# Kernel tuning notes

Measured on AMD Instinct MI355X. Metric: run time of the kernel, lower is better.

## Reference

```python
import jax, jax.numpy as jnp
import numpy as np

B, T, H, O, P, L = 128, 64, 512, 47, 4, 3
G = 4 * H


def setup_inputs() -> dict:
    key = jax.random.key(0)
    k = jax.random.split(key, 10)
    s = 0.05
    return {
        "x": jax.random.randint(k[0], (B, T), 0, O),
        "properties": jax.random.normal(k[1], (B, P), jnp.float32),
        "enc_w": jax.random.normal(k[2], (H, O), jnp.float32) * s,
        "enc_b": jnp.zeros((H,), jnp.float32),
        "dec_w": jax.random.normal(k[3], (O, H), jnp.float32) * s,
        "dec_b": jnp.zeros((O,), jnp.float32),
        "w_ih0": jax.random.normal(k[4], (G, H + P), jnp.float32) * s,
        "w_hh0": jax.random.normal(k[5], (G, H), jnp.float32) * s,
        "b_ih0": jnp.zeros((G,), jnp.float32).at[H:2 * H].set(1.0),
        "b_hh0": jnp.zeros((G,), jnp.float32).at[H:2 * H].set(1.0),
        "w_ih_rest": jax.random.normal(k[6], (L - 1, G, H), jnp.float32) * s,
        "w_hh_rest": jax.random.normal(k[7], (L - 1, G, H), jnp.float32) * s,
        "b_ih_rest": jnp.zeros((L - 1, G), jnp.float32).at[:, H:2 * H].set(1.0),
        "b_hh_rest": jnp.zeros((L - 1, G), jnp.float32).at[:, H:2 * H].set(1.0),
    }


def _lstm_cell(x, h, c, w_ih, w_hh, b_ih, b_hh):
    # torch gate order: i, f, g, o
    g = x @ w_ih.T + h @ w_hh.T + (b_ih + b_hh)
    i, f, gg, o = jnp.split(g, 4, axis=-1)
    c = jax.nn.sigmoid(f) * c + jax.nn.sigmoid(i) * jnp.tanh(gg)
    h = jax.nn.sigmoid(o) * jnp.tanh(c)
    return h, c


def reference(x, properties, enc_w, enc_b, dec_w, dec_b,
              w_ih0, w_hh0, b_ih0, b_hh0,
              w_ih_rest, w_hh_rest, b_ih_rest, b_hh_rest):
    batch = properties.shape[0]
    max_len = x.shape[1]
    n_layers = w_ih_rest.shape[0] + 1
    hidden = w_hh0.shape[1]
    out_size = dec_w.shape[0]

    # initial one-hot on symbol 1 (start token), encoded
    init = jnp.zeros((batch, out_size), properties.dtype).at[:, 1].set(1.0)
    inputs0 = init @ enc_w.T + enc_b  # [B, H]
    h0 = jnp.zeros((n_layers, batch, hidden), properties.dtype)
    c0 = jnp.zeros_like(h0)

    def step(carry, _):
        h, c, inp = carry
        xcat = jnp.concatenate([inp, properties], axis=1)  # [B, H+P]
        hs, cs = [], []
        hh, cc = _lstm_cell(xcat, h[0], c[0], w_ih0, w_hh0, b_ih0, b_hh0)
        hs.append(hh); cs.append(cc)
        for l in range(n_layers - 1):
            hh, cc = _lstm_cell(hh, h[l + 1], c[l + 1],
                                w_ih_rest[l], w_hh_rest[l],
                                b_ih_rest[l], b_hh_rest[l])
            hs.append(hh); cs.append(cc)
        logits = hh @ dec_w.T + dec_b          # [B, O]
        nxt = logits @ enc_w.T + enc_b         # feed logits back through encoder
        return (jnp.stack(hs), jnp.stack(cs), nxt), logits

    _, logits_seq = jax.lax.scan(step, (h0, c0, inputs0), None, length=max_len)
    return jnp.transpose(logits_seq, (1, 0, 2))  # [B, T, O]
```

## Files before the change

kernel.cpp:

```cpp
#include <hip/hip_runtime.h>
#include <hip/hip_fp16.h>
#include <math.h>

#define B 128
#define T 64
#define H 512
#define O 47
#define PP 4
#define G 2048
#define GH (G*H)
#define HB (H*B)


typedef _Float16 h16;
typedef _Float16 h16x2 __attribute__((ext_vector_type(2)));

__device__ __forceinline__ unsigned int pack2h(float a, float b) {
    union { unsigned int u; h16 h[2]; } c;
    c.h[0] = (h16)a; c.h[1] = (h16)b;
    return c.u;
}
__device__ __forceinline__ h16x2 as_h2(unsigned int u) {
    union { unsigned int u; h16x2 v; } c; c.u = u; return c.v;
}
__device__ __forceinline__ uint2 cload_u2(const unsigned int* p) {
    unsigned long long v = __hip_atomic_load((const unsigned long long*)p,
                                             __ATOMIC_RELAXED, __HIP_MEMORY_SCOPE_AGENT);
    union { unsigned long long u; uint2 w; } c; c.u = v; return c.w;
}
__device__ __forceinline__ void cstore_u2(unsigned int* p, uint2 v) {
    union { unsigned long long u; uint2 w; } c; c.w = v;
    __hip_atomic_store((unsigned long long*)p, c.u,
                       __ATOMIC_RELAXED, __HIP_MEMORY_SCOPE_AGENT);
}
#define FDOT2(w, x, c) __builtin_amdgcn_fdot2(as_h2(w), as_h2(x), (c), false)

#define SM_WH     0
#define SM_BIAS   12288
#define SM_DECH   14336
#define SM_BL     14592
#define SM_G      14608
#define SM_DB     22800
#define SM_H      23824
#define SM_TOTAL  24080

#define HSLOT   32768
#define NSLOT   65
#define HTOT    (3 * NSLOT * HSLOT)
#define OFF_C   HTOT
#define OFF_M   (OFF_C + 3*HB)
#define OFF_W0  (OFF_M + 4*HB)
#define OFF_BA  (OFF_W0 + 16*HB)
#define OFF_BB  (OFF_BA + 4*HB)
#define OFF_DV  (OFF_BB + 4*HB)
#define OFF_BAR (OFF_DV + 5120)
#define NEED_A  ((size_t)(OFF_BAR + 4160) * sizeof(float))

struct RnnParams {
  const float* w_hh0;
  const float* w_ihr;
  const float* w_hhr;
  const float* b_ihr;
  const float* b_hhr;
  const float* dec_w;
  const float* dec_b;
  const float* W0eff;
  const float* biasA;
  const float* biasB;
  unsigned int* h;
  float* c;
  float* out;
  unsigned int* arrive;
  unsigned int* gocnt;
};


__global__ __launch_bounds__(256) void k_init_a(
    const float* __restrict__ enc_w, const float* __restrict__ enc_b,
    const float* __restrict__ dec_b,
    unsigned int* __restrict__ h, float* __restrict__ c,
    float* __restrict__ d, float* __restrict__ nxt0,
    unsigned int* __restrict__ barptr)
{
    int idx = blockIdx.x * 256 + threadIdx.x;
    if (idx < 4160) barptr[idx] = 0u;
    if (idx < HSLOT) {
        #pragma unroll
        for (int l = 0; l < 3; ++l) h[(size_t)l * NSLOT * HSLOT + idx] = 0u;
    }
    #pragma unroll
    for (int i = 0; i < 3; ++i) c[i*HB + idx] = 0.f;
    if (idx < H) {
        float s = 0.f;
        for (int o = 0; o < O; ++o) s += enc_w[idx*O + o] * dec_b[o];
        d[idx] = enc_b[idx] + s;
        nxt0[idx] = enc_w[idx*O + 1] + enc_b[idx];
    }
}

__global__ __launch_bounds__(256) void k_init_b(
    const float* __restrict__ enc_w, const float* __restrict__ enc_b,
    const float* __restrict__ dec_b,
    float* __restrict__ h, float* __restrict__ c,
    float* __restrict__ d, float* __restrict__ nxt0,
    unsigned int* __restrict__ barptr)
{
    int idx = blockIdx.x * 256 + threadIdx.x;
    if (idx < 4160) barptr[idx] = 0u;
    #pragma unroll
    for (int i = 0; i < 3; ++i) h[i*HB + idx] = 0.f;
    #pragma unroll
    for (int i = 0; i < 3; ++i) c[i*HB + idx] = 0.f;
    if (idx < H) {
        float s = 0.f;
        for (int o = 0; o < O; ++o) s += enc_w[idx*O + o] * dec_b[o];
        d[idx] = enc_b[idx] + s;
        nxt0[idx] = enc_w[idx*O + 1] + enc_b[idx];
    }
}

__global__ __launch_bounds__(256) void k_M(
    const float* __restrict__ enc_w, const float* __restrict__ dec_w,
    float* __restrict__ M)
{
    int idx = blockIdx.x * 256 + threadIdx.x;
    int hh = idx >> 9, k = idx & 511;
    float s = 0.f;
    for (int o = 0; o < O; ++o) s += enc_w[hh*O + o] * dec_w[o*H + k];
    M[hh*H + k] = s;
}

__global__ __launch_bounds__(256) void k_cd(
    const float* __restrict__ w_ih0,
    const float* __restrict__ nxt0, const float* __restrict__ d,
    float* __restrict__ x0c, float* __restrict__ cd)
{
    int j = blockIdx.x * 256 + threadIdx.x;
    const float* row = w_ih0 + (size_t)j * (H + PP);
    float sA = 0.f, sB = 0.f;
    for (int k = 0; k < H; ++k) { float w = row[k]; sA += w * nxt0[k]; sB += w * d[k]; }
    x0c[j] = sA; cd[j] = sB;
}

__global__ __launch_bounds__(256) void k_W0eff(
    const float* __restrict__ w_ih0, const float* __restrict__ M,
    float* __restrict__ W0eff)
{
    int k0 = (threadIdx.x & 127) * 4;
    int jsub = threadIdx.x >> 7;
    int j0 = blockIdx.x * 16 + jsub * 8;
    float4 a[8];
    #pragma unroll
    for (int i = 0; i < 8; ++i) a[i] = make_float4(0.f, 0.f, 0.f, 0.f);
    for (int hh = 0; hh < H; ++hh) {
        float4 mv = *(const float4*)(M + (size_t)hh * H + k0);
        #pragma unroll
        for (int i = 0; i < 8; ++i) {
            float w = w_ih0[(size_t)(j0 + i) * (H + PP) + hh];
            a[i].x += w * mv.x; a[i].y += w * mv.y;
            a[i].z += w * mv.z; a[i].w += w * mv.w;
        }
    }
    #pragma unroll
    for (int i = 0; i < 8; ++i)
        *(float4*)(W0eff + (size_t)(j0 + i) * H + k0) = a[i];
}

__global__ __launch_bounds__(256) void k_bias(
    const float* __restrict__ w_ih0, const float* __restrict__ props,
    const float* __restrict__ b_ih0, const float* __restrict__ b_hh0,
    const float* __restrict__ x0c, const float* __restrict__ cd,
    float* __restrict__ biasA, float* __restrict__ biasB)
{
    int idx = blockIdx.x * 256 + threadIdx.x;
    int j = idx >> 7, b = idx & 127;
    const float* wp = w_ih0 + (size_t)j * (H + PP) + H;
    const float* pr = props + b * PP;
    float pc = wp[0]*pr[0] + wp[1]*pr[1] + wp[2]*pr[2] + wp[3]*pr[3];
    float base = b_ih0[j] + b_hh0[j] + pc;
    biasA[idx] = base + x0c[j];
    biasB[idx] = base + cd[j];
}


__device__ __forceinline__ void stage_weights(
    unsigned int* sWH, float* sBias, unsigned int* sDecH, float* sBL,
    const RnnParams& p, int wg, int u0, int tid, bool isdec)
{
    const float* bases[6] = { p.W0eff, p.w_hh0, p.w_ihr, p.w_hhr,
                              p.w_ihr + GH, p.w_hhr + GH };
    #pragma unroll
    for (int s = 0; s < 6; ++s) {
        for (int idx = tid; idx < 2048; idx += 512) {
            int r = idx >> 8, kp = idx & 255;
            int j = (r >> 1) * H + u0 + (r & 1);
            const float* src = bases[s] + (size_t)j * H + 2*kp;
            sWH[s*2048 + (r << 8) + kp] = pack2h(src[0], src[1]);
        }
    }
    for (int idx = tid; idx < 2048; idx += 512) {
        int pl = idx >> 10, r = (idx >> 7) & 7, b = idx & 127;
        int j = (r >> 1) * H + u0 + (r & 1);
        sBias[idx] = (pl ? p.biasB : p.biasA)[(size_t)j * B + b];
    }
    if (tid < 16) {
        int l = tid >> 3, r = tid & 7;
        int j = (r >> 1) * H + u0 + (r & 1);
        sBL[tid] = p.b_ihr[l*G + j] + p.b_hhr[l*G + j];
    }
    if (isdec && tid < 256) {
        const float* src = p.dec_w + (size_t)wg * H + 2*tid;
        sDecH[tid] = pack2h(src[0], src[1]);
    }
}


__global__ __launch_bounds__(512, 2) void rnn_persistent_a(RnnParams p)
{
    extern __shared__ float sm[];
    const int tid   = threadIdx.x;
    const int wg    = blockIdx.x;
    const int u0    = wg * 2;
    const int b4    = tid & 31;
    const int khalf = (tid >> 5) & 1;
    const int ks    = tid >> 6;

    unsigned int* sWH   = (unsigned int*)(sm + SM_WH);
    float*        sBias = sm + SM_BIAS;
    unsigned int* sDecH = (unsigned int*)(sm + SM_DECH);
    float*        sBL   = sm + SM_BL;
    float*        sG    = sm + SM_G;
    float*        sDb   = sm + SM_DB;
    float*        sH    = sm + SM_H;

    float* c0 = p.c; float* c1 = p.c + HB; float* c2 = p.c + 2*HB;
    const bool  isdec = (wg < O);
    const float decb  = isdec ? p.dec_b[wg] : 0.f;

    __builtin_amdgcn_fence(__ATOMIC_ACQUIRE, "agent");

    stage_weights(sWH, sBias, sDecH, sBL, p, wg, u0, tid, isdec);
    __syncthreads();

    unsigned int epoch = 0;
    unsigned int* arrive = p.arrive;
    unsigned int* gocnt  = p.gocnt;

    auto gbar = [&]() {
        ++epoch;
        __syncthreads();
        if (tid == 0)
            __hip_atomic_fetch_add(&arrive[(size_t)wg * 16], 1u,
                                   __ATOMIC_RELEASE, __HIP_MEMORY_SCOPE_AGENT);
        if (wg == 0) {
            if (tid < 256) {
                while (__hip_atomic_load(&arrive[(size_t)tid * 16],
                        __ATOMIC_RELAXED, __HIP_MEMORY_SCOPE_AGENT) < epoch)
                    __builtin_amdgcn_s_sleep(1);
            }
            __syncthreads();
            if (tid == 0)
                __hip_atomic_fetch_add(gocnt, 1u,
                                       __ATOMIC_RELEASE, __HIP_MEMORY_SCOPE_AGENT);
        }
        if (tid == 0) {
            while (__hip_atomic_load(gocnt, __ATOMIC_RELAXED,
                                     __HIP_MEMORY_SCOPE_AGENT) < epoch)
                __builtin_amdgcn_s_sleep(1);
        }
        __syncthreads();
    };

    auto slot = [&](int l, int s) -> unsigned int* {
        return p.h + ((size_t)(l * NSLOT + s) << 15);
    };

    auto phase = [&](const unsigned int* __restrict__ xs,
                     const unsigned int* __restrict__ hs,
                     int ph, const float* biasPlane, const float* biasScal,
                     float* cc, unsigned int* hout, bool dopig, float* dout) {
        float4 acc[8];
        #pragma unroll
        for (int r = 0; r < 8; ++r) acc[r] = make_float4(0.f, 0.f, 0.f, 0.f);
        float4 accd = make_float4(0.f, 0.f, 0.f, 0.f);

        const unsigned int* wx = sWH + (ph*2 + 0) * 2048;
        const unsigned int* wh = sWH + (ph*2 + 1) * 2048;
        const int kp0 = ks * 32 + khalf * 16;
        const int xo  = 4 * b4;

        for (int kp = kp0; kp < kp0 + 16; kp += 4) {
            uint4 x0 = *(const uint4*)(xs + (kp+0)*128 + xo);
            uint4 x1 = *(const uint4*)(xs + (kp+1)*128 + xo);
            uint4 x2 = *(const uint4*)(xs + (kp+2)*128 + xo);
            uint4 x3 = *(const uint4*)(xs + (kp+3)*128 + xo);
            #pragma unroll
            for (int r = 0; r < 8; ++r) {
                uint4 wq = *(const uint4*)(wx + r*256 + kp);
                acc[r].x = FDOT2(wq.x, x0.x, acc[r].x); acc[r].y = FDOT2(wq.x, x0.y, acc[r].y);
                acc[r].z = FDOT2(wq.x, x0.z, acc[r].z); acc[r].w = FDOT2(wq.x, x0.w, acc[r].w);
                acc[r].x = FDOT2(wq.y, x1.x, acc[r].x); acc[r].y = FDOT2(wq.y, x1.y, acc[r].y);
                acc[r].z = FDOT2(wq.y, x1.z, acc[r].z); acc[r].w = FDOT2(wq.y, x1.w, acc[r].w);
                acc[r].x = FDOT2(wq.z, x2.x, acc[r].x); acc[r].y = FDOT2(wq.z, x2.y, acc[r].y);
                acc[r].z = FDOT2(wq.z, x2.z, acc[r].z); acc[r].w = FDOT2(wq.z, x2.w, acc[r].w);
                acc[r].x = FDOT2(wq.w, x3.x, acc[r].x); acc[r].y = FDOT2(wq.w, x3.y, acc[r].y);
                acc[r].z = FDOT2(wq.w, x3.z, acc[r].z); acc[r].w = FDOT2(wq.w, x3.w, acc[r].w);
            }
            if (dopig) {
                uint4 dq = *(const uint4*)(sDecH + kp);
                accd.x = FDOT2(dq.x, x0.x, accd.x); accd.y = FDOT2(dq.x, x0.y, accd.y);
                accd.z = FDOT2(dq.x, x0.z, accd.z); accd.w = FDOT2(dq.x, x0.w, accd.w);
                accd.x = FDOT2(dq.y, x1.x, accd.x); accd.y = FDOT2(dq.y, x1.y, accd.y);
                accd.z = FDOT2(dq.y, x1.z, accd.z); accd.w = FDOT2(dq.y, x1.w, accd.w);
                accd.x = FDOT2(dq.z, x2.x, accd.x); accd.y = FDOT2(dq.z, x2.y, accd.y);
                accd.z = FDOT2(dq.z, x2.z, accd.z); accd.w = FDOT2(dq.z, x2.w, accd.w);
                accd.x = FDOT2(dq.w, x3.x, accd.x); accd.y = FDOT2(dq.w, x3.y, accd.y);
                accd.z = FDOT2(dq.w, x3.z, accd.z); accd.w = FDOT2(dq.w, x3.w, accd.w);
            }
        }
        for (int kp = kp0; kp < kp0 + 16; kp += 4) {
            uint4 x0 = *(const uint4*)(hs + (kp+0)*128 + xo);
            uint4 x1 = *(const uint4*)(hs + (kp+1)*128 + xo);
            uint4 x2 = *(const uint4*)(hs + (kp+2)*128 + xo);
            uint4 x3 = *(const uint4*)(hs + (kp+3)*128 + xo);
            #pragma unroll
            for (int r = 0; r < 8; ++r) {
                uint4 wq = *(const uint4*)(wh + r*256 + kp);
                acc[r].x = FDOT2(wq.x, x0.x, acc[r].x); acc[r].y = FDOT2(wq.x, x0.y, acc[r].y);
                acc[r].z = FDOT2(wq.x, x0.z, acc[r].z); acc[r].w = FDOT2(wq.x, x0.w, acc[r].w);
                acc[r].x = FDOT2(wq.y, x1.x, acc[r].x); acc[r].y = FDOT2(wq.y, x1.y, acc[r].y);
                acc[r].z = FDOT2(wq.y, x1.z, acc[r].z); acc[r].w = FDOT2(wq.y, x1.w, acc[r].w);
                acc[r].x = FDOT2(wq.z, x2.x, acc[r].x); acc[r].y = FDOT2(wq.z, x2.y, acc[r].y);
                acc[r].z = FDOT2(wq.z, x2.z, acc[r].z); acc[r].w = FDOT2(wq.z, x2.w, acc[r].w);
                acc[r].x = FDOT2(wq.w, x3.x, acc[r].x); acc[r].y = FDOT2(wq.w, x3.y, acc[r].y);
                acc[r].z = FDOT2(wq.w, x3.z, acc[r].z); acc[r].w = FDOT2(wq.w, x3.w, acc[r].w);
            }
        }

        #pragma unroll
        for (int r = 0; r < 8; ++r) {
            acc[r].x += __shfl_xor(acc[r].x, 32, 64);
            acc[r].y += __shfl_xor(acc[r].y, 32, 64);
            acc[r].z += __shfl_xor(acc[r].z, 32, 64);
            acc[r].w += __shfl_xor(acc[r].w, 32, 64);
        }
        if (khalf == 0) {
            #pragma unroll
            for (int r = 0; r < 8; ++r)
                *(float4*)(sG + ((r*8 + ks)*32 + b4)*4) = acc[r];
        }
        if (dopig) {
            accd.x += __shfl_xor(accd.x, 32, 64);
            accd.y += __shfl_xor(accd.y, 32, 64);
            accd.z += __shfl_xor(accd.z, 32, 64);
            accd.w += __shfl_xor(accd.w, 32, 64);
            if (khalf == 0) *(float4*)(sDb + (ks*32 + b4)*4) = accd;
        }
        __syncthreads();

        if (tid < 256) {
            int mi = tid >> 7, b = tid & 127;
            float g[4];
            #pragma unroll
            for (int q = 0; q < 4; ++q) {
                int r = q*2 + mi;
                float s = biasPlane ? biasPlane[r*128 + b] : biasScal[r];
                #pragma unroll
                for (int k2 = 0; k2 < 8; ++k2)
                    s += sG[((r*8 + k2)*32 + (b >> 2))*4 + (b & 3)];
                g[q] = s;
            }
            float ig = 1.f/(1.f+expf(-g[0]));
            float fg = 1.f/(1.f+expf(-g[1]));
            float gv = tanhf(g[2]);
            float og = 1.f/(1.f+expf(-g[3]));
            int idx = (u0 + mi)*B + b;
            float cn = fg*cc[idx] + ig*gv;
            cc[idx] = cn;
            sH[mi*128 + b] = og*tanhf(cn);
        } else if (dopig && tid < 384) {
            int b = tid - 256;
            float s = decb;
            #pragma unroll
            for (int k2 = 0; k2 < 8; ++k2)
                s += sDb[(k2*32 + (b >> 2))*4 + (b & 3)];
            dout[(size_t)b * (T*O)] = s;
        }
        __syncthreads();
        if (tid < 64) {
            int b0 = tid * 2;
            uint2 v;
            v.x = pack2h(sH[b0],     sH[128 + b0]);
            v.y = pack2h(sH[b0 + 1], sH[128 + b0 + 1]);
            cstore_u2(hout + wg*128 + b0, v);
        }
    };

    for (int t = 0; t < T; ++t) {
        bool pig = (t > 0) && isdec;
        phase(slot(2, t), slot(0, t), 0, sBias + (t == 0 ? 0 : 1024), nullptr,
              c0, slot(0, t+1), pig,
              pig ? (p.out + (size_t)(t-1)*O + wg) : nullptr);
        gbar();
        phase(slot(0, t+1), slot(1, t), 1, nullptr, sBL, c1, slot(1, t+1),
              false, nullptr);
        gbar();
        phase(slot(1, t+1), slot(2, t), 2, nullptr, sBL + 8, c2, slot(2, t+1),
              false, nullptr);
        gbar();
    }

    if (isdec) {
        const unsigned int* xs = slot(2, T);
        float4 accd = make_float4(0.f, 0.f, 0.f, 0.f);
        const int kp0 = ks * 32 + khalf * 16;
        const int xo  = 4 * b4;
        for (int kp = kp0; kp < kp0 + 16; kp += 4) {
            uint4 x0 = *(const uint4*)(xs + (kp+0)*128 + xo);
            uint4 x1 = *(const uint4*)(xs + (kp+1)*128 + xo);
            uint4 x2 = *(const uint4*)(xs + (kp+2)*128 + xo);
            uint4 x3 = *(const uint4*)(xs + (kp+3)*128 + xo);
            uint4 dq = *(const uint4*)(sDecH + kp);
            accd.x = FDOT2(dq.x, x0.x, accd.x); accd.y = FDOT2(dq.x, x0.y, accd.y);
            accd.z = FDOT2(dq.x, x0.z, accd.z); accd.w = FDOT2(dq.x, x0.w, accd.w);
            accd.x = FDOT2(dq.y, x1.x, accd.x); accd.y = FDOT2(dq.y, x1.y, accd.y);
            accd.z = FDOT2(dq.y, x1.z, accd.z); accd.w = FDOT2(dq.y, x1.w, accd.w);
            accd.x = FDOT2(dq.z, x2.x, accd.x); accd.y = FDOT2(dq.z, x2.y, accd.y);
            accd.z = FDOT2(dq.z, x2.z, accd.z); accd.w = FDOT2(dq.z, x2.w, accd.w);
            accd.x = FDOT2(dq.w, x3.x, accd.x); accd.y = FDOT2(dq.w, x3.y, accd.y);
            accd.z = FDOT2(dq.w, x3.z, accd.z); accd.w = FDOT2(dq.w, x3.w, accd.w);
        }
        accd.x += __shfl_xor(accd.x, 32, 64);
        accd.y += __shfl_xor(accd.y, 32, 64);
        accd.z += __shfl_xor(accd.z, 32, 64);
        accd.w += __shfl_xor(accd.w, 32, 64);
        if (khalf == 0) *(float4*)(sDb + (ks*32 + b4)*4) = accd;
    }
    __syncthreads();
    if (isdec && tid < 128) {
        int b = tid;
        float s = decb;
        #pragma unroll
        for (int k2 = 0; k2 < 8; ++k2)
            s += sDb[(k2*32 + (b >> 2))*4 + (b & 3)];
        p.out[((size_t)b * T + 63) * O + wg] = s;
    }
}


__global__ __launch_bounds__(512, 2) void rnn_persistent_b(RnnParams p)
{
    extern __shared__ float sm[];
    const int tid = threadIdx.x;
    const int wg  = blockIdx.x;
    const int u0  = wg * 2;
    const int b2  = tid & 63;
    const int ks  = tid >> 6;

    unsigned int* sWH   = (unsigned int*)(sm + SM_WH);
    float*        sBias = sm + SM_BIAS;
    unsigned int* sDecH = (unsigned int*)(sm + SM_DECH);
    float*        sBL   = sm + SM_BL;
    float2*       sGbuf = (float2*)(sm + SM_G);
    float2*       sDecb = (float2*)(sm + SM_DB);
    float*        sH    = sm + SM_H;

    unsigned int* h0p = p.h + 0*32768; unsigned int* h0c = p.h + 1*32768;
    unsigned int* h1p = p.h + 2*32768; unsigned int* h1c = p.h + 3*32768;
    unsigned int* h2p = p.h + 4*32768; unsigned int* h2c = p.h + 5*32768;
    float* c0 = p.c; float* c1 = p.c + HB; float* c2 = p.c + 2*HB;

    const bool  isdec = (wg < O);
    const float decb  = isdec ? p.dec_b[wg] : 0.f;

    stage_weights(sWH, sBias, sDecH, sBL, p, wg, u0, tid, isdec);
    __syncthreads();

    unsigned int epoch = 0;
    unsigned int* arrive = p.arrive;
    unsigned int* gocnt  = p.gocnt;
    auto gbar = [&]() {
        ++epoch;
        __syncthreads();
        if (tid == 0)
            __hip_atomic_fetch_add(&arrive[(size_t)wg * 16], 1u,
                                   __ATOMIC_RELEASE, __HIP_MEMORY_SCOPE_AGENT);
        if (wg == 0) {
            if (tid < 256) {
                while (__hip_atomic_load(&arrive[(size_t)tid * 16],
                        __ATOMIC_RELAXED, __HIP_MEMORY_SCOPE_AGENT) < epoch)
                    __builtin_amdgcn_s_sleep(1);
            }
            __syncthreads();
            if (tid == 0)
                __hip_atomic_fetch_add(gocnt, 1u,
                                       __ATOMIC_RELEASE, __HIP_MEMORY_SCOPE_AGENT);
        }
        if (tid == 0) {
            while (__hip_atomic_load(gocnt, __ATOMIC_RELAXED,
                                     __HIP_MEMORY_SCOPE_AGENT) < epoch)
                __builtin_amdgcn_s_sleep(1);
        }
        __syncthreads();
    };

    auto phase = [&](const unsigned int* __restrict__ xs,
                     const unsigned int* __restrict__ hs,
                     int ph, const float* biasPlane, const float* biasScal,
                     float* cc, unsigned int* hout, bool dopig, float* dout) {
        float2 acc[8];
        #pragma unroll
        for (int r = 0; r < 8; ++r) { acc[r].x = 0.f; acc[r].y = 0.f; }
        float2 accd; accd.x = 0.f; accd.y = 0.f;

        const unsigned int* wx = sWH + (ph*2 + 0) * 2048;
        const unsigned int* wh = sWH + (ph*2 + 1) * 2048;
        const int kb = ks * 32;
        const int xo = 2 * b2;

        for (int kp = kb; kp < kb + 32; kp += 4) {
            uint2 x0 = cload_u2(xs + (kp+0)*128 + xo);
            uint2 x1 = cload_u2(xs + (kp+1)*128 + xo);
            uint2 x2 = cload_u2(xs + (kp+2)*128 + xo);
            uint2 x3 = cload_u2(xs + (kp+3)*128 + xo);
            if (dopig) {
                uint4 dq = *(const uint4*)(sDecH + kp);
                accd.x = FDOT2(dq.x, x0.x, accd.x); accd.y = FDOT2(dq.x, x0.y, accd.y);
                accd.x = FDOT2(dq.y, x1.x, accd.x); accd.y = FDOT2(dq.y, x1.y, accd.y);
                accd.x = FDOT2(dq.z, x2.x, accd.x); accd.y = FDOT2(dq.z, x2.y, accd.y);
                accd.x = FDOT2(dq.w, x3.x, accd.x); accd.y = FDOT2(dq.w, x3.y, accd.y);
            }
            #pragma unroll
            for (int r = 0; r < 8; ++r) {
                uint4 wq = *(const uint4*)(wx + r*256 + kp);
                acc[r].x = FDOT2(wq.x, x0.x, acc[r].x); acc[r].y = FDOT2(wq.x, x0.y, acc[r].y);
                acc[r].x = FDOT2(wq.y, x1.x, acc[r].x); acc[r].y = FDOT2(wq.y, x1.y, acc[r].y);
                acc[r].x = FDOT2(wq.z, x2.x, acc[r].x); acc[r].y = FDOT2(wq.z, x2.y, acc[r].y);
                acc[r].x = FDOT2(wq.w, x3.x, acc[r].x); acc[r].y = FDOT2(wq.w, x3.y, acc[r].y);
            }
        }
        for (int kp = kb; kp < kb + 32; kp += 4) {
            uint2 x0 = cload_u2(hs + (kp+0)*128 + xo);
            uint2 x1 = cload_u2(hs + (kp+1)*128 + xo);
            uint2 x2 = cload_u2(hs + (kp+2)*128 + xo);
            uint2 x3 = cload_u2(hs + (kp+3)*128 + xo);
            #pragma unroll
            for (int r = 0; r < 8; ++r) {
                uint4 wq = *(const uint4*)(wh + r*256 + kp);
                acc[r].x = FDOT2(wq.x, x0.x, acc[r].x); acc[r].y = FDOT2(wq.x, x0.y, acc[r].y);
                acc[r].x = FDOT2(wq.y, x1.x, acc[r].x); acc[r].y = FDOT2(wq.y, x1.y, acc[r].y);
                acc[r].x = FDOT2(wq.z, x2.x, acc[r].x); acc[r].y = FDOT2(wq.z, x2.y, acc[r].y);
                acc[r].x = FDOT2(wq.w, x3.x, acc[r].x); acc[r].y = FDOT2(wq.w, x3.y, acc[r].y);
            }
        }

        #pragma unroll
        for (int r = 0; r < 8; ++r) sGbuf[(r*8 + ks)*64 + b2] = acc[r];
        if (dopig) sDecb[ks*64 + b2] = accd;
        __syncthreads();

        if (tid < 256) {
            int mi = tid >> 7, b = tid & 127;
            float g[4];
            #pragma unroll
            for (int q = 0; q < 4; ++q) {
                int r = q*2 + mi;
                float s = biasPlane ? biasPlane[r*128 + b] : biasScal[r];
                #pragma unroll
                for (int k2 = 0; k2 < 8; ++k2) {
                    float2 v = sGbuf[(r*8 + k2)*64 + (b >> 1)];
                    s += (b & 1) ? v.y : v.x;
                }
                g[q] = s;
            }
            float ig = 1.f/(1.f+expf(-g[0]));
            float fg = 1.f/(1.f+expf(-g[1]));
            float gv = tanhf(g[2]);
            float og = 1.f/(1.f+expf(-g[3]));
            int idx = (u0 + mi)*B + b;
            float cn = fg*cc[idx] + ig*gv;
            cc[idx] = cn;
            sH[mi*128 + b] = og*tanhf(cn);
        } else if (dopig && tid < 384) {
            int b = tid - 256;
            float s = decb;
            #pragma unroll
            for (int k2 = 0; k2 < 8; ++k2) {
                float2 v = sDecb[k2*64 + (b >> 1)];
                s += (b & 1) ? v.y : v.x;
            }
            dout[(size_t)b * (T*O)] = s;
        }
        __syncthreads();
        if (tid < 64) {
            int b0 = tid * 2;
            uint2 v;
            v.x = pack2h(sH[b0],     sH[128 + b0]);
            v.y = pack2h(sH[b0 + 1], sH[128 + b0 + 1]);
            cstore_u2(hout + wg*128 + b0, v);
        }
    };

    for (int t = 0; t < T; ++t) {
        bool pig = (t > 0) && isdec;
        phase(h2p, h0p, 0, sBias + (t == 0 ? 0 : 1024), nullptr,
              c0, h0c, pig, pig ? (p.out + (size_t)(t-1)*O + wg) : nullptr);
        gbar();
        phase(h0c, h1p, 1, nullptr, sBL, c1, h1c, false, nullptr);
        gbar();
        phase(h1c, h2p, 2, nullptr, sBL + 8, c2, h2c, false, nullptr);
        gbar();
        unsigned int* tp;
        tp = h0p; h0p = h0c; h0c = tp;
        tp = h1p; h1p = h1c; h1c = tp;
        tp = h2p; h2p = h2c; h2c = tp;
    }

    if (isdec) {
        float2 accd; accd.x = 0.f; accd.y = 0.f;
        const int kb = ks * 32;
        const int xo = 2 * b2;
        for (int kp = kb; kp < kb + 32; kp += 4) {
            uint2 x0 = cload_u2(h2p + (kp+0)*128 + xo);
            uint2 x1 = cload_u2(h2p + (kp+1)*128 + xo);
            uint2 x2 = cload_u2(h2p + (kp+2)*128 + xo);
            uint2 x3 = cload_u2(h2p + (kp+3)*128 + xo);
            uint4 dq = *(const uint4*)(sDecH + kp);
            accd.x = FDOT2(dq.x, x0.x, accd.x); accd.y = FDOT2(dq.x, x0.y, accd.y);
            accd.x = FDOT2(dq.y, x1.x, accd.x); accd.y = FDOT2(dq.y, x1.y, accd.y);
            accd.x = FDOT2(dq.z, x2.x, accd.x); accd.y = FDOT2(dq.z, x2.y, accd.y);
            accd.x = FDOT2(dq.w, x3.x, accd.x); accd.y = FDOT2(dq.w, x3.y, accd.y);
        }
        sDecb[ks*64 + b2] = accd;
    }
    __syncthreads();
    if (isdec && tid < 128) {
        int b = tid;
        float s = decb;
        #pragma unroll
        for (int k2 = 0; k2 < 8; ++k2) {
            float2 v = sDecb[k2*64 + (b >> 1)];
            s += (b & 1) ? v.y : v.x;
        }
        p.out[((size_t)b * T + 63) * O + wg] = s;
    }
}


__global__ __launch_bounds__(256) void init_kernel(
    const float* __restrict__ enc_w, const float* __restrict__ enc_b,
    float* __restrict__ nxtT, float* __restrict__ hbufs, float* __restrict__ cbufs)
{
    int idx = blockIdx.x * 256 + threadIdx.x;
    #pragma unroll
    for (int i = 0; i < 6; ++i) hbufs[i * HB + idx] = 0.f;
    #pragma unroll
    for (int i = 0; i < 3; ++i) cbufs[i * HB + idx] = 0.f;
    int h = idx >> 7;
    nxtT[idx] = enc_w[h * O + 1] + enc_b[h];
}

__global__ __launch_bounds__(256) void transpose_kernel(
    const float* __restrict__ dec_w, const float* __restrict__ enc_w,
    float* __restrict__ dec_wT, float* __restrict__ enc_wT)
{
    int idx = blockIdx.x * 256 + threadIdx.x;
    if (idx < O * H) {
        int o = idx / H, k = idx - o * H;
        dec_wT[k * O + o] = dec_w[o * H + k];
        enc_wT[o * H + k] = enc_w[k * O + o];
    }
}

__global__ __launch_bounds__(512) void gates_kernel(
    const float* __restrict__ xT, const float* __restrict__ hT,
    const float* __restrict__ w_ih, int ldih,
    const float* __restrict__ w_hh,
    const float* __restrict__ b_ih, const float* __restrict__ b_hh,
    const float* __restrict__ props,
    float* __restrict__ c, float* __restrict__ hout)
{
    const int wg = blockIdx.x;
    const int bg = wg >> 7, jg = wg & 127;
    const int m0 = jg * 4;
    const int lane_b = threadIdx.x & 63, ks = threadIdx.x >> 6;
    const int bb = (bg << 6) + lane_b;
    float acc[16];
    #pragma unroll
    for (int r = 0; r < 16; ++r) acc[r] = 0.f;
    const float* wih_rows[16]; const float* whh_rows[16];
    #pragma unroll
    for (int q = 0; q < 4; ++q)
        #pragma unroll
        for (int mi = 0; mi < 4; ++mi) {
            int r = q * 4 + mi, j = q * H + m0 + mi;
            wih_rows[r] = w_ih + (size_t)j * ldih;
            whh_rows[r] = w_hh + (size_t)j * H;
        }
    const int kbeg = ks * 64, kend = ks * 64 + 64;
    for (int k0 = kbeg; k0 < kend; k0 += 4) {
        float x0 = xT[(k0+0)*B+bb], x1 = xT[(k0+1)*B+bb];
        float x2 = xT[(k0+2)*B+bb], x3 = xT[(k0+3)*B+bb];
        #pragma unroll
        for (int r = 0; r < 16; ++r) {
            float4 wv = *(const float4*)(wih_rows[r] + k0);
            acc[r] += wv.x*x0 + wv.y*x1 + wv.z*x2 + wv.w*x3;
        }
    }
    for (int k0 = kbeg; k0 < kend; k0 += 4) {
        float x0 = hT[(k0+0)*B+bb], x1 = hT[(k0+1)*B+bb];
        float x2 = hT[(k0+2)*B+bb], x3 = hT[(k0+3)*B+bb];
        #pragma unroll
        for (int r = 0; r < 16; ++r) {
            float4 wv = *(const float4*)(whh_rows[r] + k0);
            acc[r] += wv.x*x0 + wv.y*x1 + wv.z*x2 + wv.w*x3;
        }
    }
    __shared__ float gbuf[16][8][64];
    #pragma unroll
    for (int r = 0; r < 16; ++r) gbuf[r][ks][lane_b] = acc[r];
    __syncthreads();
    if (threadIdx.x < 256) {
        int mi = threadIdx.x >> 6, b = threadIdx.x & 63;
        int bbo = (bg << 6) + b, m = m0 + mi;
        float g[4];
        #pragma unroll
        for (int q = 0; q < 4; ++q) {
            int j = q * H + m;
            float s = b_ih[j] + b_hh[j];
            #pragma unroll
            for (int k2 = 0; k2 < 8; ++k2) s += gbuf[q*4+mi][k2][b];
            if (props) {
                const float* wp = w_ih + (size_t)j * ldih + H;
                const float* pp = props + bbo * PP;
                s += wp[0]*pp[0] + wp[1]*pp[1] + wp[2]*pp[2] + wp[3]*pp[3];
            }
            g[q] = s;
        }
        float ig = 1.f/(1.f+expf(-g[0]));
        float fg = 1.f/(1.f+expf(-g[1]));
        float gv = tanhf(g[2]);
        float og = 1.f/(1.f+expf(-g[3]));
        int idx = m * B + bbo;
        float cn = fg * c[idx] + ig * gv;
        c[idx] = cn;
        hout[idx] = og * tanhf(cn);
    }
}

__global__ __launch_bounds__(256) void decenc_kernel(
    const float* __restrict__ h2T, const float* __restrict__ dec_wT,
    const float* __restrict__ dec_b, const float* __restrict__ enc_wT,
    const float* __restrict__ enc_b, float* __restrict__ nxtT,
    float* __restrict__ out, int t)
{
    const int b = blockIdx.x;
    const int w = threadIdx.x >> 6, o = threadIdx.x & 63;
    __shared__ float red[4][64];
    __shared__ float lg[64];
    float p = 0.f;
    if (o < O)
        for (int k = w * 128; k < w * 128 + 128; ++k)
            p += h2T[k * B + b] * dec_wT[k * O + o];
    red[w][o] = p;
    __syncthreads();
    if (threadIdx.x < 64) {
        int oo = threadIdx.x;
        float s = 0.f;
        if (oo < O) {
            s = dec_b[oo] + red[0][oo] + red[1][oo] + red[2][oo] + red[3][oo];
            out[((size_t)b * T + t) * O + oo] = s;
        }
        lg[oo] = s;
    }
    __syncthreads();
    for (int h = threadIdx.x; h < H; h += 256) {
        float s = enc_b[h];
        #pragma unroll 1
        for (int oo = 0; oo < O; ++oo) s += lg[oo] * enc_wT[oo * H + h];
        nxtT[h * B + b] = s;
    }
}

extern "C" void kernel_launch(void* const* d_in, const int* in_sizes, int n_in,
                              void* d_out, int out_size, void* d_ws, size_t ws_size,
                              hipStream_t stream) {
    const float* props = (const float*)d_in[1];
    const float* enc_w = (const float*)d_in[2];
    const float* enc_b = (const float*)d_in[3];
    const float* dec_w = (const float*)d_in[4];
    const float* dec_b = (const float*)d_in[5];
    const float* w_ih0 = (const float*)d_in[6];
    const float* w_hh0 = (const float*)d_in[7];
    const float* b_ih0 = (const float*)d_in[8];
    const float* b_hh0 = (const float*)d_in[9];
    const float* w_ihr = (const float*)d_in[10];
    const float* w_hhr = (const float*)d_in[11];
    const float* b_ihr = (const float*)d_in[12];
    const float* b_hhr = (const float*)d_in[13];

    float* ws = (float*)d_ws;
    const size_t NEED_B = ((size_t)34 * HB + 5120 + 4160) * sizeof(float);
    const size_t LDS_BYTES = (size_t)SM_TOTAL * sizeof(float);

    static int lds_a = -1, lds_b = -1;
    if (lds_a < 0) {
        lds_a = (hipFuncSetAttribute((const void*)rnn_persistent_a,
                  hipFuncAttributeMaxDynamicSharedMemorySize,
                  (int)LDS_BYTES) == hipSuccess) ? 1 : 0;
        lds_b = (hipFuncSetAttribute((const void*)rnn_persistent_b,
                  hipFuncAttributeMaxDynamicSharedMemorySize,
                  (int)LDS_BYTES) == hipSuccess) ? 1 : 0;
    }

    if (ws_size >= NEED_A && lds_a == 1) {
        unsigned int* hbuf = (unsigned int*)ws;
        float* cbuf  = ws + OFF_C;
        float* M     = ws + OFF_M;
        float* W0eff = ws + OFF_W0;
        float* biasA = ws + OFF_BA;
        float* biasB = ws + OFF_BB;
        float* dvec  = ws + OFF_DV;
        float* nxt0  = dvec + 512;
        float* x0c   = nxt0 + 512;
        float* cd    = x0c + 2048;
        unsigned int* barptr = (unsigned int*)(ws + OFF_BAR);

        k_init_a<<<256, 256, 0, stream>>>(enc_w, enc_b, dec_b, hbuf, cbuf,
                                          dvec, nxt0, barptr);
        k_M<<<1024, 256, 0, stream>>>(enc_w, dec_w, M);
        k_cd<<<8, 256, 0, stream>>>(w_ih0, nxt0, dvec, x0c, cd);
        k_W0eff<<<128, 256, 0, stream>>>(w_ih0, M, W0eff);
        k_bias<<<1024, 256, 0, stream>>>(w_ih0, props, b_ih0, b_hh0, x0c, cd,
                                         biasA, biasB);

        RnnParams prm;
        prm.w_hh0 = w_hh0; prm.w_ihr = w_ihr; prm.w_hhr = w_hhr;
        prm.b_ihr = b_ihr; prm.b_hhr = b_hhr;
        prm.dec_w = dec_w; prm.dec_b = dec_b;
        prm.W0eff = W0eff; prm.biasA = biasA; prm.biasB = biasB;
        prm.h = hbuf; prm.c = cbuf; prm.out = (float*)d_out;
        prm.arrive = barptr; prm.gocnt = barptr + 4096;

        void* args[] = { &prm };
        hipLaunchCooperativeKernel((const void*)rnn_persistent_a,
                                   dim3(256), dim3(512), args,
                                   (unsigned int)LDS_BYTES, stream);
        return;
    }

    if (ws_size >= NEED_B && lds_b == 1) {
        unsigned int* hbuf = (unsigned int*)ws;
        float* cbuf  = ws + 3*HB;
        float* M     = ws + 6*HB;
        float* W0eff = ws + 10*HB;
        float* biasA = ws + 26*HB;
        float* biasB = ws + 30*HB;
        float* dvec  = ws + 34*HB;
        float* nxt0  = dvec + 512;
        float* x0c   = nxt0 + 512;
        float* cd    = x0c + 2048;
        unsigned int* barptr = (unsigned int*)(cd + 2048);

        k_init_b<<<256, 256, 0, stream>>>(enc_w, enc_b, dec_b, (float*)hbuf,
                                          cbuf, dvec, nxt0, barptr);
        k_M<<<1024, 256, 0, stream>>>(enc_w, dec_w, M);
        k_cd<<<8, 256, 0, stream>>>(w_ih0, nxt0, dvec, x0c, cd);
        k_W0eff<<<128, 256, 0, stream>>>(w_ih0, M, W0eff);
        k_bias<<<1024, 256, 0, stream>>>(w_ih0, props, b_ih0, b_hh0, x0c, cd,
                                         biasA, biasB);

        RnnParams prm;
        prm.w_hh0 = w_hh0; prm.w_ihr = w_ihr; prm.w_hhr = w_hhr;
        prm.b_ihr = b_ihr; prm.b_hhr = b_hhr;
        prm.dec_w = dec_w; prm.dec_b = dec_b;
        prm.W0eff = W0eff; prm.biasA = biasA; prm.biasB = biasB;
        prm.h = hbuf; prm.c = cbuf; prm.out = (float*)d_out;
        prm.arrive = barptr; prm.gocnt = barptr + 4096;

        void* args[] = { &prm };
        hipLaunchCooperativeKernel((const void*)rnn_persistent_b,
                                   dim3(256), dim3(512), args,
                                   (unsigned int)LDS_BYTES, stream);
        return;
    }

    float* nxtT   = ws;
    float* hb     = ws + HB;
    float* cb     = ws + 7*HB;
    float* dec_wT = ws + 10*HB;
    float* enc_wT = dec_wT + H*O;

    init_kernel<<<256, 256, 0, stream>>>(enc_w, enc_b, nxtT, hb, cb);
    transpose_kernel<<<(O*H + 255)/256, 256, 0, stream>>>(dec_w, enc_w, dec_wT, enc_wT);

    float* hprev[3]; float* hcur[3];
    for (int l = 0; l < 3; ++l) { hprev[l] = hb + (2*l)*HB; hcur[l] = hb + (2*l+1)*HB; }

    for (int t = 0; t < T; ++t) {
        gates_kernel<<<256, 512, 0, stream>>>(nxtT, hprev[0], w_ih0, H+PP, w_hh0,
                                              b_ih0, b_hh0, props, cb, hcur[0]);
        gates_kernel<<<256, 512, 0, stream>>>(hcur[0], hprev[1], w_ihr, H, w_hhr,
                                              b_ihr, b_hhr, nullptr, cb + HB, hcur[1]);
        gates_kernel<<<256, 512, 0, stream>>>(hcur[1], hprev[2], w_ihr + (size_t)G*H, H,
                                              w_hhr + (size_t)G*H, b_ihr + G, b_hhr + G,
                                              nullptr, cb + 2*HB, hcur[2]);
        decenc_kernel<<<B, 256, 0, stream>>>(hcur[2], dec_wT, dec_b, enc_wT, enc_b,
                                             nxtT, (float*)d_out, t);
        for (int l = 0; l < 3; ++l) { float* tp = hprev[l]; hprev[l] = hcur[l]; hcur[l] = tp; }
    }
}
```

Before: 2.323 ms.

## Split grid barrier into arrive/wait and overlap recurrent matmul with barrier

Replaces the centralized two-level grid barrier (workgroup 0 gathers arrivals, then releases everyone through a go counter) with a split arrive/wait barrier in which every workgroup polls all 256 arrival counters itself. Each phase now computes the recurrent h·W_hh part before waiting, since it only depends on the previous timestep's state, and does the input part and gate math after the wait. This moves independent work into the barrier latency and removes one round trip through workgroup 0. The cost is that every workgroup polls 256 counters, which adds atomic traffic, and correctness now relies on the slot layout keeping previous-step state valid during the wait.

```diff
diff --git a/kernel.cpp b/kernel.cpp
--- a/kernel.cpp
+++ b/kernel.cpp
@@ -242,53 +242,64 @@
     stage_weights(sWH, sBias, sDecH, sBL, p, wg, u0, tid, isdec);
     __syncthreads();
 
-    unsigned int epoch = 0;
+    unsigned int done = 0;
     unsigned int* arrive = p.arrive;
-    unsigned int* gocnt  = p.gocnt;
-
-    auto gbar = [&]() {
-        ++epoch;
+
+    auto bar_wait = [&]() {
+        if (tid < 256) {
+            while (__hip_atomic_load(&arrive[(size_t)tid * 16],
+                    __ATOMIC_RELAXED, __HIP_MEMORY_SCOPE_AGENT) < done)
+                __builtin_amdgcn_s_sleep(1);
+        }
+        __syncthreads();
+    };
+    auto bar_arrive = [&]() {
         __syncthreads();
         if (tid == 0)
             __hip_atomic_fetch_add(&arrive[(size_t)wg * 16], 1u,
                                    __ATOMIC_RELEASE, __HIP_MEMORY_SCOPE_AGENT);
-        if (wg == 0) {
-            if (tid < 256) {
-                while (__hip_atomic_load(&arrive[(size_t)tid * 16],
-                        __ATOMIC_RELAXED, __HIP_MEMORY_SCOPE_AGENT) < epoch)
-                    __builtin_amdgcn_s_sleep(1);
-            }
-            __syncthreads();
-            if (tid == 0)
-                __hip_atomic_fetch_add(gocnt, 1u,
-                                       __ATOMIC_RELEASE, __HIP_MEMORY_SCOPE_AGENT);
-        }
-        if (tid == 0) {
-            while (__hip_atomic_load(gocnt, __ATOMIC_RELAXED,
-                                     __HIP_MEMORY_SCOPE_AGENT) < epoch)
-                __builtin_amdgcn_s_sleep(1);
-        }
-        __syncthreads();
+        ++done;
     };
 
     auto slot = [&](int l, int s) -> unsigned int* {
         return p.h + ((size_t)(l * NSLOT + s) << 15);
     };
 
-    auto phase = [&](const unsigned int* __restrict__ xs,
-                     const unsigned int* __restrict__ hs,
-                     int ph, const float* biasPlane, const float* biasScal,
-                     float* cc, unsigned int* hout, bool dopig, float* dout) {
-        float4 acc[8];
+    const int kp0 = ks * 32 + khalf * 16;
+    const int xo  = 4 * b4;
+
+    float4 acc[8];
+
+    auto h_part = [&](const unsigned int* __restrict__ hs, int ph) {
         #pragma unroll
         for (int r = 0; r < 8; ++r) acc[r] = make_float4(0.f, 0.f, 0.f, 0.f);
+        const unsigned int* wh = sWH + (ph*2 + 1) * 2048;
+        for (int kp = kp0; kp < kp0 + 16; kp += 4) {
+            uint4 x0 = *(const uint4*)(hs + (kp+0)*128 + xo);
+            uint4 x1 = *(const uint4*)(hs + (kp+1)*128 + xo);
+            uint4 x2 = *(const uint4*)(hs + (kp+2)*128 + xo);
+            uint4 x3 = *(const uint4*)(hs + (kp+3)*128 + xo);
+            #pragma unroll
+            for (int r = 0; r < 8; ++r) {
+                uint4 wq = *(const uint4*)(wh + r*256 + kp);
+                acc[r].x = FDOT2(wq.x, x0.x, acc[r].x); acc[r].y = FDOT2(wq.x, x0.y, acc[r].y);
+                acc[r].z = FDOT2(wq.x, x0.z, acc[r].z); acc[r].w = FDOT2(wq.x, x0.w, acc[r].w);
+                acc[r].x = FDOT2(wq.y, x1.x, acc[r].x); acc[r].y = FDOT2(wq.y, x1.y, acc[r].y);
+                acc[r].z = FDOT2(wq.y, x1.z, acc[r].z); acc[r].w = FDOT2(wq.y, x1.w, acc[r].w);
+                acc[r].x = FDOT2(wq.z, x2.x, acc[r].x); acc[r].y = FDOT2(wq.z, x2.y, acc[r].y);
+                acc[r].z = FDOT2(wq.z, x2.z, acc[r].z); acc[r].w = FDOT2(wq.z, x2.w, acc[r].w);
+                acc[r].x = FDOT2(wq.w, x3.x, acc[r].x); acc[r].y = FDOT2(wq.w, x3.y, acc[r].y);
+                acc[r].z = FDOT2(wq.w, x3.z, acc[r].z); acc[r].w = FDOT2(wq.w, x3.w, acc[r].w);
+            }
+        }
+    };
+
+    auto x_part_finish = [&](const unsigned int* __restrict__ xs, int ph,
+                             const float* biasPlane, const float* biasScal,
+                             float* cc, unsigned int* hout,
+                             bool dopig, float* dout) {
         float4 accd = make_float4(0.f, 0.f, 0.f, 0.f);
-
         const unsigned int* wx = sWH + (ph*2 + 0) * 2048;
-        const unsigned int* wh = sWH + (ph*2 + 1) * 2048;
-        const int kp0 = ks * 32 + khalf * 16;
-        const int xo  = 4 * b4;
-
         for (int kp = kp0; kp < kp0 + 16; kp += 4) {
             uint4 x0 = *(const uint4*)(xs + (kp+0)*128 + xo);
             uint4 x1 = *(const uint4*)(xs + (kp+1)*128 + xo);
@@ -318,24 +329,6 @@
                 accd.z = FDOT2(dq.w, x3.z, accd.z); accd.w = FDOT2(dq.w, x3.w, accd.w);
             }
         }
-        for (int kp = kp0; kp < kp0 + 16; kp += 4) {
-            uint4 x0 = *(const uint4*)(hs + (kp+0)*128 + xo);
-            uint4 x1 = *(const uint4*)(hs + (kp+1)*128 + xo);
-            uint4 x2 = *(const uint4*)(hs + (kp+2)*128 + xo);
-            uint4 x3 = *(const uint4*)(hs + (kp+3)*128 + xo);
-            #pragma unroll
-            for (int r = 0; r < 8; ++r) {
-                uint4 wq = *(const uint4*)(wh + r*256 + kp);
-                acc[r].x = FDOT2(wq.x, x0.x, acc[r].x); acc[r].y = FDOT2(wq.x, x0.y, acc[r].y);
-                acc[r].z = FDOT2(wq.x, x0.z, acc[r].z); acc[r].w = FDOT2(wq.x, x0.w, acc[r].w);
-                acc[r].x = FDOT2(wq.y, x1.x, acc[r].x); acc[r].y = FDOT2(wq.y, x1.y, acc[r].y);
-                acc[r].z = FDOT2(wq.y, x1.z, acc[r].z); acc[r].w = FDOT2(wq.y, x1.w, acc[r].w);
-                acc[r].x = FDOT2(wq.z, x2.x, acc[r].x); acc[r].y = FDOT2(wq.z, x2.y, acc[r].y);
-                acc[r].z = FDOT2(wq.z, x2.z, acc[r].z); acc[r].w = FDOT2(wq.z, x2.w, acc[r].w);
-                acc[r].x = FDOT2(wq.w, x3.x, acc[r].x); acc[r].y = FDOT2(wq.w, x3.y, acc[r].y);
-                acc[r].z = FDOT2(wq.w, x3.z, acc[r].z); acc[r].w = FDOT2(wq.w, x3.w, acc[r].w);
-            }
-        }
 
         #pragma unroll
         for (int r = 0; r < 8; ++r) {
@@ -398,23 +391,28 @@
 
     for (int t = 0; t < T; ++t) {
         bool pig = (t > 0) && isdec;
-        phase(slot(2, t), slot(0, t), 0, sBias + (t == 0 ? 0 : 1024), nullptr,
-              c0, slot(0, t+1), pig,
-              pig ? (p.out + (size_t)(t-1)*O + wg) : nullptr);
-        gbar();
-        phase(slot(0, t+1), slot(1, t), 1, nullptr, sBL, c1, slot(1, t+1),
-              false, nullptr);
-        gbar();
-        phase(slot(1, t+1), slot(2, t), 2, nullptr, sBL + 8, c2, slot(2, t+1),
-              false, nullptr);
-        gbar();
-    }
-
+        h_part(slot(0, t), 0);
+        bar_wait();
+        x_part_finish(slot(2, t), 0, sBias + (t == 0 ? 0 : 1024), nullptr,
+                      c0, slot(0, t+1), pig,
+                      pig ? (p.out + (size_t)(t-1)*O + wg) : nullptr);
+        bar_arrive();
+        h_part(slot(1, t), 1);
+        bar_wait();
+        x_part_finish(slot(0, t+1), 1, nullptr, sBL, c1, slot(1, t+1),
+                      false, nullptr);
+        bar_arrive();
+        h_part(slot(2, t), 2);
+        bar_wait();
+        x_part_finish(slot(1, t+1), 2, nullptr, sBL + 8, c2, slot(2, t+1),
+                      false, nullptr);
+        bar_arrive();
+    }
+
+    bar_wait();
     if (isdec) {
         const unsigned int* xs = slot(2, T);
         float4 accd = make_float4(0.f, 0.f, 0.f, 0.f);
-        const int kp0 = ks * 32 + khalf * 16;
-        const int xo  = 4 * b4;
         for (int kp = kp0; kp < kp0 + 16; kp += 4) {
             uint4 x0 = *(const uint4*)(xs + (kp+0)*128 + xo);
             uint4 x1 = *(const uint4*)(xs + (kp+1)*128 + xo);
```

Measured after the change: 4.554 ms. 1.96x slower.

## Split batch into two halves with split-phase grid barriers to overlap sync

Applied to the files above, without the earlier changes.

Each layer phase of the persistent LSTM kernel is split into two batch halves, each with its own arrive/go counters. Barriers are split into separate arrive and wait steps, so the wait for one half's barrier can overlap with computing the other half. The inner K loop per thread shrinks to 8 and an extra shuffle stage is added to the reduction. In exchange, the number of barrier operations per timestep doubles and each phase does half the work, which raises fixed overhead.

```diff
diff --git a/kernel.cpp b/kernel.cpp
--- a/kernel.cpp
+++ b/kernel.cpp
@@ -54,7 +54,8 @@
 #define OFF_BB  (OFF_BA + 4*HB)
 #define OFF_DV  (OFF_BB + 4*HB)
 #define OFF_BAR (OFF_DV + 5120)
-#define NEED_A  ((size_t)(OFF_BAR + 4160) * sizeof(float))
+#define BAR_UINTS 8256
+#define NEED_A  ((size_t)(OFF_BAR + BAR_UINTS) * sizeof(float))
 
 struct RnnParams {
   const float* w_hh0;
@@ -83,7 +84,7 @@
     unsigned int* __restrict__ barptr)
 {
     int idx = blockIdx.x * 256 + threadIdx.x;
-    if (idx < 4160) barptr[idx] = 0u;
+    if (idx < BAR_UINTS) barptr[idx] = 0u;
     if (idx < HSLOT) {
         #pragma unroll
         for (int l = 0; l < 3; ++l) h[(size_t)l * NSLOT * HSLOT + idx] = 0u;
@@ -218,12 +219,13 @@
 __global__ __launch_bounds__(512, 2) void rnn_persistent_a(RnnParams p)
 {
     extern __shared__ float sm[];
-    const int tid   = threadIdx.x;
-    const int wg    = blockIdx.x;
-    const int u0    = wg * 2;
-    const int b4    = tid & 31;
-    const int khalf = (tid >> 5) & 1;
-    const int ks    = tid >> 6;
+    const int tid = threadIdx.x;
+    const int wg  = blockIdx.x;
+    const int u0  = wg * 2;
+    const int b16 = tid & 15;
+    const int kq  = (tid >> 4) & 3;
+    const int ks  = tid >> 6;
+    const int kp0 = ks * 32 + kq * 8;
 
     unsigned int* sWH   = (unsigned int*)(sm + SM_WH);
     float*        sBias = sm + SM_BIAS;
@@ -242,43 +244,47 @@
     stage_weights(sWH, sBias, sDecH, sBL, p, wg, u0, tid, isdec);
     __syncthreads();
 
-    unsigned int epoch = 0;
-    unsigned int* arrive = p.arrive;
-    unsigned int* gocnt  = p.gocnt;
-
-    auto gbar = [&]() {
-        ++epoch;
+    unsigned int done0 = 0, done1 = 0;
+    unsigned int* arr[2] = { p.arrive, p.arrive + 4096 };
+    unsigned int* go[2]  = { p.gocnt,  p.gocnt + 16 };
+
+    auto bar_wait = [&](int s) {
+        unsigned int d = s ? done1 : done0;
+        if (tid == 0) {
+            while (__hip_atomic_load(go[s], __ATOMIC_RELAXED,
+                                     __HIP_MEMORY_SCOPE_AGENT) < d)
+                __builtin_amdgcn_s_sleep(1);
+        }
+        __syncthreads();
+    };
+    auto bar_arrive = [&](int s) {
         __syncthreads();
         if (tid == 0)
-            __hip_atomic_fetch_add(&arrive[(size_t)wg * 16], 1u,
+            __hip_atomic_fetch_add(&arr[s][(size_t)wg * 16], 1u,
                                    __ATOMIC_RELEASE, __HIP_MEMORY_SCOPE_AGENT);
+        unsigned int d = (s ? ++done1 : ++done0);
         if (wg == 0) {
             if (tid < 256) {
-                while (__hip_atomic_load(&arrive[(size_t)tid * 16],
-                        __ATOMIC_RELAXED, __HIP_MEMORY_SCOPE_AGENT) < epoch)
+                while (__hip_atomic_load(&arr[s][(size_t)tid * 16],
+                        __ATOMIC_RELAXED, __HIP_MEMORY_SCOPE_AGENT) < d)
                     __builtin_amdgcn_s_sleep(1);
             }
             __syncthreads();
             if (tid == 0)
-                __hip_atomic_fetch_add(gocnt, 1u,
+                __hip_atomic_fetch_add(go[s], 1u,
                                        __ATOMIC_RELEASE, __HIP_MEMORY_SCOPE_AGENT);
         }
-        if (tid == 0) {
-            while (__hip_atomic_load(gocnt, __ATOMIC_RELAXED,
-                                     __HIP_MEMORY_SCOPE_AGENT) < epoch)
-                __builtin_amdgcn_s_sleep(1);
-        }
-        __syncthreads();
     };
 
     auto slot = [&](int l, int s) -> unsigned int* {
         return p.h + ((size_t)(l * NSLOT + s) << 15);
     };
 
-    auto phase = [&](const unsigned int* __restrict__ xs,
-                     const unsigned int* __restrict__ hs,
-                     int ph, const float* biasPlane, const float* biasScal,
-                     float* cc, unsigned int* hout, bool dopig, float* dout) {
+    auto phase_s = [&](int s,
+                       const unsigned int* __restrict__ xs,
+                       const unsigned int* __restrict__ hs,
+                       int ph, const float* biasPlane, const float* biasScal,
+                       float* cc, unsigned int* hout, bool dopig, float* dout) {
         float4 acc[8];
         #pragma unroll
         for (int r = 0; r < 8; ++r) acc[r] = make_float4(0.f, 0.f, 0.f, 0.f);
@@ -286,10 +292,9 @@
 
         const unsigned int* wx = sWH + (ph*2 + 0) * 2048;
         const unsigned int* wh = sWH + (ph*2 + 1) * 2048;
-        const int kp0 = ks * 32 + khalf * 16;
-        const int xo  = 4 * b4;
-
-        for (int kp = kp0; kp < kp0 + 16; kp += 4) {
+        const int xo = 4 * b16 + 64 * s;
+
+        for (int kp = kp0; kp < kp0 + 8; kp += 4) {
             uint4 x0 = *(const uint4*)(xs + (kp+0)*128 + xo);
             uint4 x1 = *(const uint4*)(xs + (kp+1)*128 + xo);
             uint4 x2 = *(const uint4*)(xs + (kp+2)*128 + xo);
@@ -318,7 +323,7 @@
                 accd.z = FDOT2(dq.w, x3.z, accd.z); accd.w = FDOT2(dq.w, x3.w, accd.w);
             }
         }
-        for (int kp = kp0; kp < kp0 + 16; kp += 4) {
+        for (int kp = kp0; kp < kp0 + 8; kp += 4) {
             uint4 x0 = *(const uint4*)(hs + (kp+0)*128 + xo);
             uint4 x1 = *(const uint4*)(hs + (kp+1)*128 + xo);
             uint4 x2 = *(const uint4*)(hs + (kp+2)*128 + xo);
@@ -339,36 +344,45 @@
 
         #pragma unroll
         for (int r = 0; r < 8; ++r) {
+            acc[r].x += __shfl_xor(acc[r].x, 16, 64);
+            acc[r].y += __shfl_xor(acc[r].y, 16, 64);
+            acc[r].z += __shfl_xor(acc[r].z, 16, 64);
+            acc[r].w += __shfl_xor(acc[r].w, 16, 64);
             acc[r].x += __shfl_xor(acc[r].x, 32, 64);
             acc[r].y += __shfl_xor(acc[r].y, 32, 64);
             acc[r].z += __shfl_xor(acc[r].z, 32, 64);
             acc[r].w += __shfl_xor(acc[r].w, 32, 64);
         }
-        if (khalf == 0) {
+        if (kq == 0) {
             #pragma unroll
             for (int r = 0; r < 8; ++r)
-                *(float4*)(sG + ((r*8 + ks)*32 + b4)*4) = acc[r];
+                *(float4*)(sG + ((r*8 + ks)*16 + b16)*4) = acc[r];
         }
         if (dopig) {
+            accd.x += __shfl_xor(accd.x, 16, 64);
+            accd.y += __shfl_xor(accd.y, 16, 64);
+            accd.z += __shfl_xor(accd.z, 16, 64);
+            accd.w += __shfl_xor(accd.w, 16, 64);
             accd.x += __shfl_xor(accd.x, 32, 64);
             accd.y += __shfl_xor(accd.y, 32, 64);
             accd.z += __shfl_xor(accd.z, 32, 64);
             accd.w += __shfl_xor(accd.w, 32, 64);
-            if (khalf == 0) *(float4*)(sDb + (ks*32 + b4)*4) = accd;
+            if (kq == 0) *(float4*)(sDb + (ks*16 + b16)*4) = accd;
         }
         __syncthreads();
 
-        if (tid < 256) {
-            int mi = tid >> 7, b = tid & 127;
+        if (tid < 128) {
+            int mi = tid >> 6, bl = tid & 63;
+            int b = 64*s + bl;
             float g[4];
             #pragma unroll
             for (int q = 0; q < 4; ++q) {
                 int r = q*2 + mi;
-                float s = biasPlane ? biasPlane[r*128 + b] : biasScal[r];
+                float sgv = biasPlane ? biasPlane[r*128 + b] : biasScal[r];
                 #pragma unroll
                 for (int k2 = 0; k2 < 8; ++k2)
-                    s += sG[((r*8 + k2)*32 + (b >> 2))*4 + (b & 3)];
-                g[q] = s;
+                    sgv += sG[(r*8 + k2)*64 + bl];
+                g[q] = sgv;
             }
             float ig = 1.f/(1.f+expf(-g[0]));
             float fg = 1.f/(1.f+expf(-g[1]));
@@ -377,49 +391,67 @@
             int idx = (u0 + mi)*B + b;
             float cn = fg*cc[idx] + ig*gv;
             cc[idx] = cn;
-            sH[mi*128 + b] = og*tanhf(cn);
-        } else if (dopig && tid < 384) {
-            int b = tid - 256;
-            float s = decb;
+            sH[mi*64 + bl] = og*tanhf(cn);
+        } else if (dopig && tid < 192) {
+            int bl = tid - 128;
+            float sv = decb;
             #pragma unroll
-            for (int k2 = 0; k2 < 8; ++k2)
-                s += sDb[(k2*32 + (b >> 2))*4 + (b & 3)];
-            dout[(size_t)b * (T*O)] = s;
+            for (int k2 = 0; k2 < 8; ++k2) sv += sDb[k2*64 + bl];
+            dout[(size_t)(64*s + bl) * (T*O)] = sv;
         }
         __syncthreads();
-        if (tid < 64) {
+        if (tid < 32) {
             int b0 = tid * 2;
             uint2 v;
-            v.x = pack2h(sH[b0],     sH[128 + b0]);
-            v.y = pack2h(sH[b0 + 1], sH[128 + b0 + 1]);
-            cstore_u2(hout + wg*128 + b0, v);
+            v.x = pack2h(sH[b0],     sH[64 + b0]);
+            v.y = pack2h(sH[b0 + 1], sH[64 + b0 + 1]);
+            cstore_u2(hout + wg*128 + 64*s + b0, v);
         }
     };
 
     for (int t = 0; t < T; ++t) {
         bool pig = (t > 0) && isdec;
-        phase(slot(2, t), slot(0, t), 0, sBias + (t == 0 ? 0 : 1024), nullptr,
-              c0, slot(0, t+1), pig,
-              pig ? (p.out + (size_t)(t-1)*O + wg) : nullptr);
-        gbar();
-        phase(slot(0, t+1), slot(1, t), 1, nullptr, sBL, c1, slot(1, t+1),
-              false, nullptr);
-        gbar();
-        phase(slot(1, t+1), slot(2, t), 2, nullptr, sBL + 8, c2, slot(2, t+1),
-              false, nullptr);
-        gbar();
-    }
-
+        const float* bp0 = sBias + (t == 0 ? 0 : 1024);
+        bar_wait(0);
+        phase_s(0, slot(2, t), slot(0, t), 0, bp0, nullptr, c0, slot(0, t+1),
+                pig, pig ? (p.out + (size_t)(t-1)*O + wg) : nullptr);
+        bar_arrive(0);
+        bar_wait(1);
+        phase_s(1, slot(2, t), slot(0, t), 0, bp0, nullptr, c0, slot(0, t+1),
+                pig, pig ? (p.out + (size_t)(t-1)*O + wg) : nullptr);
+        bar_arrive(1);
+        bar_wait(0);
+        phase_s(0, slot(0, t+1), slot(1, t), 1, nullptr, sBL, c1, slot(1, t+1),
+                false, nullptr);
+        bar_arrive(0);
+        bar_wait(1);
+        phase_s(1, slot(0, t+1), slot(1, t), 1, nullptr, sBL, c1, slot(1, t+1),
+                false, nullptr);
+        bar_arrive(1);
+        bar_wait(0);
+        phase_s(0, slot(1, t+1), slot(2, t), 2, nullptr, sBL + 8, c2, slot(2, t+1),
+                false, nullptr);
+        bar_arrive(0);
+        bar_wait(1);
+        phase_s(1, slot(1, t+1), slot(2, t), 2, nullptr, sBL + 8, c2, slot(2, t+1),
+                false, nullptr);
+        bar_arrive(1);
+    }
+
+    bar_wait(0);
+    bar_wait(1);
     if (isdec) {
         const unsigned int* xs = slot(2, T);
+        const int b4f = tid & 31;
+        const int khf = (tid >> 5) & 1;
+        const int kpf = ks * 32 + khf * 16;
+        const int xof = 4 * b4f;
         float4 accd = make_float4(0.f, 0.f, 0.f, 0.f);
-        const int kp0 = ks * 32 + khalf * 16;
-        const int xo  = 4 * b4;
-        for (int kp = kp0; kp < kp0 + 16; kp += 4) {
-            uint4 x0 = *(const uint4*)(xs + (kp+0)*128 + xo);
-            uint4 x1 = *(const uint4*)(xs + (kp+1)*128 + xo);
-            uint4 x2 = *(const uint4*)(xs + (kp+2)*128 + xo);
-            uint4 x3 = *(const uint4*)(xs + (kp+3)*128 + xo);
+        for (int kp = kpf; kp < kpf + 16; kp += 4) {
+            uint4 x0 = *(const uint4*)(xs + (kp+0)*128 + xof);
+            uint4 x1 = *(const uint4*)(xs + (kp+1)*128 + xof);
+            uint4 x2 = *(const uint4*)(xs + (kp+2)*128 + xof);
+            uint4 x3 = *(const uint4*)(xs + (kp+3)*128 + xof);
             uint4 dq = *(const uint4*)(sDecH + kp);
             accd.x = FDOT2(dq.x, x0.x, accd.x); accd.y = FDOT2(dq.x, x0.y, accd.y);
             accd.z = FDOT2(dq.x, x0.z, accd.z); accd.w = FDOT2(dq.x, x0.w, accd.w);
@@ -434,7 +466,7 @@
         accd.y += __shfl_xor(accd.y, 32, 64);
         accd.z += __shfl_xor(accd.z, 32, 64);
         accd.w += __shfl_xor(accd.w, 32, 64);
-        if (khalf == 0) *(float4*)(sDb + (ks*32 + b4)*4) = accd;
+        if (khf == 0) *(float4*)(sDb + (ks*32 + b4f)*4) = accd;
     }
     __syncthreads();
     if (isdec && tid < 128) {
@@ -840,7 +872,7 @@
         prm.dec_w = dec_w; prm.dec_b = dec_b;
         prm.W0eff = W0eff; prm.biasA = biasA; prm.biasB = biasB;
         prm.h = hbuf; prm.c = cbuf; prm.out = (float*)d_out;
-        prm.arrive = barptr; prm.gocnt = barptr + 4096;
+        prm.arrive = barptr; prm.gocnt = barptr + 8192;
 
         void* args[] = { &prm };
         hipLaunchCooperativeKernel((const void*)rnn_persistent_a,
```

Measured after the change: 3.607 ms. +55.3%, slower.
